# Kernel optimization log

Measured on AMD Instinct MI355X. Metric: run time of the kernel, lower is better.

The kernel has to match this reference:

```python
import jax, jax.numpy as jnp
import numpy as np

B, T, D_MODEL, N_HEADS, N_KV = 2, 2048, 1024, 16, 4
HEAD = D_MODEL // N_HEADS  # 64
NEG_INF = -1e9


def sine_table(features, length):
    # standard RoPE frequency table: theta_i = 10000^(2i/d)
    fraction = jnp.arange(0, features, 2, dtype=jnp.float32) / features
    timescale = 10000.0 ** fraction  # (features/2,)
    sinusoid = jnp.arange(length, dtype=jnp.float32)[:, None] / timescale[None, :]
    sinusoid = jnp.concatenate([sinusoid, sinusoid], axis=-1)  # (L, features)
    return jnp.sin(sinusoid), jnp.cos(sinusoid)


def rotate_half(x):
    x1, x2 = jnp.split(x, 2, axis=-1)
    return jnp.concatenate([-x2, x1], axis=-1)


def apply_rope(x, sin, cos):
    # x: (B, H, T, D); sin/cos: (L, D)
    t = x.shape[-2]
    return x * cos[:t][None, None] + rotate_half(x) * sin[:t][None, None]


def setup_inputs() -> dict:
    key = jax.random.key(0)
    k1, k2, k3, k4 = jax.random.split(key, 4)
    return {
        'q': jax.random.normal(k1, (B, T, D_MODEL), dtype=jnp.float32),
        'k': jax.random.normal(k2, (B, T, N_KV * HEAD), dtype=jnp.float32),
        'v': jax.random.normal(k3, (B, T, N_KV * HEAD), dtype=jnp.float32),
        'w_out': jax.random.normal(k4, (D_MODEL, D_MODEL), dtype=jnp.float32) * 0.02,
    }


def reference(q, k, v, w_out):
    Bq, Tq, C = q.shape
    head = C // N_HEADS
    # split heads: q -> (B, n_heads, T, head); k/v -> (B, n_kv, T, head)
    qh = q.reshape(Bq, Tq, N_HEADS, head).transpose(0, 2, 1, 3)
    kh = k.reshape(Bq, Tq, N_KV, head).transpose(0, 2, 1, 3)
    vh = v.reshape(Bq, Tq, N_KV, head).transpose(0, 2, 1, 3)
    # inline RoPE on q and k
    sin, cos = sine_table(head, Tq)
    qh = apply_rope(qh, sin, cos)
    kh = apply_rope(kh, sin, cos)
    # GQA repeat of kv heads to match q heads
    rep = N_HEADS // N_KV
    kh = jnp.repeat(kh, rep, axis=1)
    vh = jnp.repeat(vh, rep, axis=1)
    # manual scaled-dot-product attention with causal masking (full T^2 logits)
    logits = jnp.einsum('bhqd,bhkd->bhqk', qh, kh) / jnp.sqrt(jnp.float32(head))
    causal = jnp.tril(jnp.ones((Tq, Tq), dtype=jnp.float32))
    logits = jnp.where(causal == 0, NEG_INF, logits)
    attn = jax.nn.softmax(logits, axis=-1)
    out = jnp.einsum('bhqk,bhkd->bhqd', attn, vh)
    out = out.transpose(0, 2, 1, 3).reshape(Bq, Tq, C)
    return out @ w_out
```

## Files before the change

kernel.cpp:

```cpp
#include <hip/hip_runtime.h>
#include <math.h>

#define T_SEQ 2048
#define NH    16
#define NKV   4

typedef __attribute__((ext_vector_type(8))) _Float16 f16x8;
typedef __attribute__((ext_vector_type(4))) _Float16 f16x4;
typedef __attribute__((ext_vector_type(4))) float    f32x4;

__global__ __launch_bounds__(256) void prep_kernel(const float* __restrict__ k,
                                                   const float* __restrict__ v,
                                                   const float* __restrict__ w,
                                                   float2* __restrict__ tb,
                                                   _Float16* __restrict__ Kr,
                                                   _Float16* __restrict__ Vt,
                                                   _Float16* __restrict__ Wt)
{
    __shared__ _Float16 L[64 * 72];
    const int bx = blockIdx.x;
    if (bx < 256) {
        int idx = bx * 256 + threadIdx.x;
        int i = idx & 31, t = idx >> 5;
        float inv = __expf((float)i * (-9.210340371976184f / 32.0f));
        float ang = (float)t * inv;
        tb[idx] = make_float2(cosf(ang), sinf(ang));
    } else if (bx < 2304) {
        int idx = (bx - 256) * 256 + threadIdx.x;
        int i   = idx & 31;
        int t   = (idx >> 5) & 2047;
        int bk  = idx >> 16;
        float inv = __expf((float)i * (-9.210340371976184f / 32.0f));
        float ang = (float)t * inv;
        float sn = sinf(ang), cs = cosf(ang);
        const float* src = k + ((size_t)(bk >> 2) * T_SEQ + t) * 256 + (bk & 3) * 64 + i;
        float x1 = src[0], x2 = src[32];
        _Float16* dst = Kr + ((size_t)bk * T_SEQ + t) * 64 + i;
        dst[0]  = (_Float16)(x1 * cs - x2 * sn);
        dst[32] = (_Float16)(x2 * cs + x1 * sn);
    } else if (bx < 2560) {
        const int id = bx - 2304;
        const int t0 = (id & 31) * 64, bk = id >> 5;
        const int b = bk >> 2, kh = bk & 3;
        const int rr = threadIdx.x >> 2, pp = threadIdx.x & 3;
        const float* src = v + ((size_t)(b * T_SEQ + t0 + rr)) * 256 + kh * 64 + pp * 16;
        f32x4 s0 = *(const f32x4*)(src), s1 = *(const f32x4*)(src + 4);
        f32x4 s2 = *(const f32x4*)(src + 8), s3 = *(const f32x4*)(src + 12);
        _Float16* lp = &L[rr * 72 + pp * 16];
        #pragma unroll
        for (int j = 0; j < 4; ++j) { lp[j] = (_Float16)s0[j]; lp[4+j] = (_Float16)s1[j];
                                      lp[8+j] = (_Float16)s2[j]; lp[12+j] = (_Float16)s3[j]; }
        __syncthreads();
        f16x8 w0, w1;
        #pragma unroll
        for (int j = 0; j < 8; ++j) w0[j] = L[(pp * 16 + j) * 72 + rr];
        #pragma unroll
        for (int j = 0; j < 8; ++j) w1[j] = L[(pp * 16 + 8 + j) * 72 + rr];
        _Float16* dst = Vt + ((size_t)bk * 64 + rr) * T_SEQ + t0 + pp * 16;
        *(f16x8*)dst = w0; *(f16x8*)(dst + 8) = w1;
    } else {
        const int id = bx - 2560;
        const int k0 = (id & 15) * 64, n0 = (id >> 4) * 64;
        const int rr = threadIdx.x >> 2, pp = threadIdx.x & 3;
        const float* src = w + (size_t)(k0 + rr) * 1024 + n0 + pp * 16;
        f32x4 s0 = *(const f32x4*)(src), s1 = *(const f32x4*)(src + 4);
        f32x4 s2 = *(const f32x4*)(src + 8), s3 = *(const f32x4*)(src + 12);
        _Float16* lp = &L[rr * 72 + pp * 16];
        #pragma unroll
        for (int j = 0; j < 4; ++j) { lp[j] = (_Float16)s0[j]; lp[4+j] = (_Float16)s1[j];
                                      lp[8+j] = (_Float16)s2[j]; lp[12+j] = (_Float16)s3[j]; }
        __syncthreads();
        f16x8 w0, w1;
        #pragma unroll
        for (int j = 0; j < 8; ++j) w0[j] = L[(pp * 16 + j) * 72 + rr];
        #pragma unroll
        for (int j = 0; j < 8; ++j) w1[j] = L[(pp * 16 + 8 + j) * 72 + rr];
        _Float16* dst = Wt + (size_t)(n0 + rr) * 1024 + k0 + pp * 16;
        *(f16x8*)dst = w0; *(f16x8*)(dst + 8) = w1;
    }
}


__global__ __launch_bounds__(256) void attn_kernel(const float* __restrict__ q,
                                                   const float2* __restrict__ tb,
                                                   const _Float16* __restrict__ Kr,
                                                   const _Float16* __restrict__ Vt,
                                                   _Float16* __restrict__ AO)
{
    __shared__ _Float16 smem[16384];

    const int wid  = threadIdx.x >> 6;
    const int lane = threadIdx.x & 63;
    const int bh = blockIdx.x & 31;
    const int p  = blockIdx.x >> 5;
    const int qb0 = p, qb1 = 31 - p;
    const int b = bh >> 4, h = bh & 15;
    const int kh = h >> 2;
    const int bkh = b * NKV + kh;
    const int g = lane >> 4, r = lane & 15;

    const int srow   = wid * 16 + (lane >> 3);
    const int schunk = lane & 7;
    const _Float16* kgbase = Kr + (size_t)bkh * T_SEQ * 64;
    const _Float16* vgbase = Vt + (size_t)bkh * 64 * T_SEQ;
    const int kd0 = srow * 64 + ((schunk ^ (srow & 7)) * 8);
    const int kd1 = kd0 + 8 * 64;

    f16x8 stK0, stK1, stV0, stV1;
    {
        const _Float16* kg = kgbase + (size_t)srow * 64 + schunk * 8;
        stK0 = *(const f16x8*)(kg);
        stK1 = *(const f16x8*)(kg + 8 * 64);
        const _Float16* vg = vgbase + (size_t)srow * T_SEQ + schunk * 8;
        stV0 = *(const f16x8*)(vg);
        stV1 = *(const f16x8*)(vg + 8 * T_SEQ);
    }

    f16x8 qa[2][2];
    #pragma unroll
    for (int tl = 0; tl < 2; ++tl) {
        const int t = (tl ? qb1 : qb0) * 64 + wid * 16 + r;
        const float* qs = q + ((size_t)b * T_SEQ + t) * 1024 + h * 64 + 8 * g;
        const float2* tp = tb + t * 32 + 8 * g;
        #pragma unroll
        for (int j = 0; j < 8; ++j) {
            float x0 = qs[j], x1 = qs[32 + j];
            float2 cs = tp[j];
            qa[tl][0][j] = (_Float16)((x0 * cs.x - x1 * cs.y) * 0.125f);
            qa[tl][1][j] = (_Float16)((x1 * cs.x + x0 * cs.y) * 0.125f);
        }
    }

    *(f16x8*)(&smem[kd0])        = stK0;
    *(f16x8*)(&smem[kd1])        = stK1;
    *(f16x8*)(&smem[8192 + kd0]) = stV0;
    *(f16x8*)(&smem[8192 + kd1]) = stV1;
    __syncthreads();

    f32x4 o[2][4];
    f32x4 o4[2];
    #pragma unroll
    for (int tl = 0; tl < 2; ++tl) {
        #pragma unroll
        for (int db = 0; db < 4; ++db) o[tl][db] = (f32x4){0.f,0.f,0.f,0.f};
        o4[tl] = (f32x4){0.f,0.f,0.f,0.f};
    }
    const f16x4 onesf = {(_Float16)1.f, (_Float16)1.f, (_Float16)1.f, (_Float16)1.f};
    float mrun[2] = {-INFINITY, -INFINITY};
    int cur = 0;

    for (int kvb = 0; kvb <= qb1; ++kvb) {
        const bool hasNext = (kvb < qb1);
        if (hasNext) {
            const int nb = (kvb + 1) * 64;
            const _Float16* kg = kgbase + (size_t)(nb + srow) * 64 + schunk * 8;
            stK0 = *(const f16x8*)(kg);
            stK1 = *(const f16x8*)(kg + 8 * 64);
            const _Float16* vg = vgbase + (size_t)srow * T_SEQ + nb + schunk * 8;
            stV0 = *(const f16x8*)(vg);
            stV1 = *(const f16x8*)(vg + 8 * T_SEQ);
        }
        const bool act0 = (kvb <= qb0);
        const _Float16* ks = smem + cur * 4096;
        const _Float16* vs = smem + 8192 + cur * 4096;

        f32x4 stt[2][4];
        __builtin_amdgcn_s_setprio(1);
        #pragma unroll
        for (int kt = 0; kt < 4; ++kt) {
            f16x8 ka0 = *(const f16x8*)(ks + (kt*16 + r) * 64 + ((g       ^ (r & 7)) * 8));
            f16x8 ka1 = *(const f16x8*)(ks + (kt*16 + r) * 64 + (((4 + g) ^ (r & 7)) * 8));
            f32x4 s1 = {0.f,0.f,0.f,0.f};
            s1 = __builtin_amdgcn_mfma_f32_16x16x32_f16(ka0, qa[1][0], s1, 0, 0, 0);
            s1 = __builtin_amdgcn_mfma_f32_16x16x32_f16(ka1, qa[1][1], s1, 0, 0, 0);
            stt[1][kt] = s1;
            if (act0) {
                f32x4 s0 = {0.f,0.f,0.f,0.f};
                s0 = __builtin_amdgcn_mfma_f32_16x16x32_f16(ka0, qa[0][0], s0, 0, 0, 0);
                s0 = __builtin_amdgcn_mfma_f32_16x16x32_f16(ka1, qa[0][1], s0, 0, 0, 0);
                stt[0][kt] = s0;
            }
        }
        __builtin_amdgcn_s_setprio(0);

        if (kvb == qb0) {
            #pragma unroll
            for (int kt = 0; kt < 4; ++kt)
                #pragma unroll
                for (int j = 0; j < 4; ++j)
                    if (kt*16 + 4*g + j > wid*16 + r) stt[0][kt][j] = -1e9f;
        }
        if (kvb == qb1) {
            #pragma unroll
            for (int kt = 0; kt < 4; ++kt)
                #pragma unroll
                for (int j = 0; j < 4; ++j)
                    if (kt*16 + 4*g + j > wid*16 + r) stt[1][kt][j] = -1e9f;
        }

        f16x4 pf[2][4];
        #pragma unroll
        for (int tl = 0; tl < 2; ++tl) {
            if (tl == 0 && !act0) continue;
            float a0 = fmaxf(fmaxf(stt[tl][0][0], stt[tl][0][1]),
                             fmaxf(stt[tl][0][2], stt[tl][0][3]));
            float a1 = fmaxf(fmaxf(stt[tl][1][0], stt[tl][1][1]),
                             fmaxf(stt[tl][1][2], stt[tl][1][3]));
            float a2 = fmaxf(fmaxf(stt[tl][2][0], stt[tl][2][1]),
                             fmaxf(stt[tl][2][2], stt[tl][2][3]));
            float a3 = fmaxf(fmaxf(stt[tl][3][0], stt[tl][3][1]),
                             fmaxf(stt[tl][3][2], stt[tl][3][3]));
            float pmL = fmaxf(fmaxf(a0, a1), fmaxf(a2, a3));
            if (!__all(pmL <= mrun[tl] + 8.0f)) {
                float pm = fmaxf(pmL, __shfl_xor(pmL, 16));
                pm = fmaxf(pm, __shfl_xor(pm, 32));
                float mn   = fmaxf(mrun[tl], pm);
                float corr = __expf(mrun[tl] - mn);
                mrun[tl]   = mn;
                f32x4 cf = { __shfl(corr, 4*g + 0), __shfl(corr, 4*g + 1),
                             __shfl(corr, 4*g + 2), __shfl(corr, 4*g + 3) };
                o[tl][0] *= cf; o[tl][1] *= cf; o[tl][2] *= cf; o[tl][3] *= cf;
                o4[tl]   *= cf;
            }
            #pragma unroll
            for (int kt = 0; kt < 4; ++kt) {
                float p0 = __expf(stt[tl][kt][0] - mrun[tl]);
                float p1 = __expf(stt[tl][kt][1] - mrun[tl]);
                float p2 = __expf(stt[tl][kt][2] - mrun[tl]);
                float p3 = __expf(stt[tl][kt][3] - mrun[tl]);
                pf[tl][kt] = (f16x4){(_Float16)p0, (_Float16)p1,
                                     (_Float16)p2, (_Float16)p3};
            }
        }

        __builtin_amdgcn_s_setprio(1);
        #pragma unroll
        for (int kt = 0; kt < 4; ++kt) {
            const int vc = ((2*kt + (g >> 1)) ^ (r & 7)) * 8 + (g & 1) * 4;
            f16x4 v0 = *(const f16x4*)(vs + (0*16 + r) * 64 + vc);
            f16x4 v1 = *(const f16x4*)(vs + (1*16 + r) * 64 + vc);
            f16x4 v2 = *(const f16x4*)(vs + (2*16 + r) * 64 + vc);
            f16x4 v3 = *(const f16x4*)(vs + (3*16 + r) * 64 + vc);
            o[1][0] = __builtin_amdgcn_mfma_f32_16x16x16f16(pf[1][kt], v0, o[1][0], 0, 0, 0);
            o[1][1] = __builtin_amdgcn_mfma_f32_16x16x16f16(pf[1][kt], v1, o[1][1], 0, 0, 0);
            o[1][2] = __builtin_amdgcn_mfma_f32_16x16x16f16(pf[1][kt], v2, o[1][2], 0, 0, 0);
            o[1][3] = __builtin_amdgcn_mfma_f32_16x16x16f16(pf[1][kt], v3, o[1][3], 0, 0, 0);
            o4[1]   = __builtin_amdgcn_mfma_f32_16x16x16f16(pf[1][kt], onesf, o4[1], 0, 0, 0);
            if (act0) {
                o[0][0] = __builtin_amdgcn_mfma_f32_16x16x16f16(pf[0][kt], v0, o[0][0], 0, 0, 0);
                o[0][1] = __builtin_amdgcn_mfma_f32_16x16x16f16(pf[0][kt], v1, o[0][1], 0, 0, 0);
                o[0][2] = __builtin_amdgcn_mfma_f32_16x16x16f16(pf[0][kt], v2, o[0][2], 0, 0, 0);
                o[0][3] = __builtin_amdgcn_mfma_f32_16x16x16f16(pf[0][kt], v3, o[0][3], 0, 0, 0);
                o4[0]   = __builtin_amdgcn_mfma_f32_16x16x16f16(pf[0][kt], onesf, o4[0], 0, 0, 0);
            }
        }
        __builtin_amdgcn_s_setprio(0);

        if (hasNext) {
            _Float16* kw = smem + (cur ^ 1) * 4096;
            _Float16* vw = smem + 8192 + (cur ^ 1) * 4096;
            *(f16x8*)(&kw[kd0]) = stK0;
            *(f16x8*)(&kw[kd1]) = stK1;
            *(f16x8*)(&vw[kd0]) = stV0;
            *(f16x8*)(&vw[kd1]) = stV1;
            cur ^= 1;
        }
        __syncthreads();
    }

    #pragma unroll
    for (int tl = 0; tl < 2; ++tl) {
        f32x4 li;
        #pragma unroll
        for (int j = 0; j < 4; ++j) li[j] = 1.0f / o4[tl][j];
        _Float16* Os = smem + tl * 4608;
        #pragma unroll
        for (int db = 0; db < 4; ++db) {
            f32x4 ov = o[tl][db] * li;
            #pragma unroll
            for (int j = 0; j < 4; ++j)
                Os[(wid*16 + 4*g + j) * 72 + db*16 + r] = (_Float16)ov[j];
        }
    }
    __syncthreads();
    {
        const int row = threadIdx.x >> 2, part = threadIdx.x & 3;
        #pragma unroll
        for (int tl = 0; tl < 2; ++tl) {
            const int qb = tl ? qb1 : qb0;
            const _Float16* src = smem + tl * 4608 + row * 72 + part * 16;
            _Float16* dst = AO + ((size_t)b * T_SEQ + qb * 64 + row) * 1024 + h * 64 + part * 16;
            *(f16x8*)dst       = *(const f16x8*)src;
            *(f16x8*)(dst + 8) = *(const f16x8*)(src + 8);
        }
    }
}


#define AST 40
__global__ __launch_bounds__(256) void gemm_kernel(const _Float16* __restrict__ A,
                                                   const _Float16* __restrict__ Bt,
                                                   float* __restrict__ C)
{
    __shared__ _Float16 As[2][128 * AST];
    __shared__ _Float16 Bs[2][64 * AST];
    const int tid  = threadIdx.x;
    const int by   = blockIdx.x & 31;
    const int bx   = blockIdx.x >> 5;
    const int lane = tid & 63;
    const int wid  = tid >> 6;
    const int g = lane >> 4, r = lane & 15;
    const int wm = wid >> 1, wn = wid & 1;

    f32x4 acc[4][2];
    #pragma unroll
    for (int i = 0; i < 4; ++i)
        #pragma unroll
        for (int j = 0; j < 2; ++j) acc[i][j] = (f32x4){0.f,0.f,0.f,0.f};

    const int c0 = tid, c1 = tid + 256;
    const size_t a0off = (size_t)(by*128 + (c0 >> 2)) * 1024 + (c0 & 3) * 8;
    const size_t a1off = (size_t)(by*128 + (c1 >> 2)) * 1024 + (c1 & 3) * 8;
    const size_t b0off = (size_t)(bx*64  + (c0 >> 2)) * 1024 + (c0 & 3) * 8;
    const int ad0 = (c0 >> 2) * AST + (c0 & 3) * 8;
    const int ad1 = (c1 >> 2) * AST + (c1 & 3) * 8;

    f16x8 a0 = *(const f16x8*)(A  + a0off);
    f16x8 a1 = *(const f16x8*)(A  + a1off);
    f16x8 b0 = *(const f16x8*)(Bt + b0off);
    *(f16x8*)(&As[0][ad0]) = a0;
    *(f16x8*)(&As[0][ad1]) = a1;
    *(f16x8*)(&Bs[0][ad0]) = b0;
    __syncthreads();
    int cur = 0;

    for (int kt = 0; kt < 32; ++kt) {
        if (kt < 31) {
            a0 = *(const f16x8*)(A  + a0off + (kt+1) * 32);
            a1 = *(const f16x8*)(A  + a1off + (kt+1) * 32);
            b0 = *(const f16x8*)(Bt + b0off + (kt+1) * 32);
        }
        f16x8 af[4], bfv[2];
        #pragma unroll
        for (int mi = 0; mi < 4; ++mi)
            af[mi] = *(const f16x8*)(&As[cur][(wm*64 + mi*16 + r) * AST + 8 * g]);
        #pragma unroll
        for (int ni = 0; ni < 2; ++ni)
            bfv[ni] = *(const f16x8*)(&Bs[cur][(wn*32 + ni*16 + r) * AST + 8 * g]);
        __builtin_amdgcn_s_setprio(1);
        #pragma unroll
        for (int mi = 0; mi < 4; ++mi)
            #pragma unroll
            for (int ni = 0; ni < 2; ++ni)
                acc[mi][ni] = __builtin_amdgcn_mfma_f32_16x16x32_f16(
                                  af[mi], bfv[ni], acc[mi][ni], 0, 0, 0);
        __builtin_amdgcn_s_setprio(0);
        if (kt < 31) {
            *(f16x8*)(&As[cur ^ 1][ad0]) = a0;
            *(f16x8*)(&As[cur ^ 1][ad1]) = a1;
            *(f16x8*)(&Bs[cur ^ 1][ad0]) = b0;
            cur ^= 1;
        }
        __syncthreads();
    }
    #pragma unroll
    for (int mi = 0; mi < 4; ++mi)
        #pragma unroll
        for (int ni = 0; ni < 2; ++ni)
            #pragma unroll
            for (int j = 0; j < 4; ++j)
                C[(size_t)(by*128 + wm*64 + mi*16 + 4*g + j) * 1024
                  + bx*64 + wn*32 + ni*16 + r] = acc[mi][ni][j];
}


extern "C" void kernel_launch(void* const* d_in, const int* in_sizes, int n_in,
                              void* d_out, int out_size, void* d_ws, size_t ws_size,
                              hipStream_t stream) {
    const float* q = (const float*)d_in[0];
    const float* k = (const float*)d_in[1];
    const float* v = (const float*)d_in[2];
    const float* w = (const float*)d_in[3];
    float* out = (float*)d_out;

    char* ws = (char*)d_ws;
    float2*   tb = (float2*)(ws);
    _Float16* Kr = (_Float16*)(ws + ((size_t)1 << 20));
    _Float16* Vt = (_Float16*)(ws + ((size_t)3 << 20));
    _Float16* Wt = (_Float16*)(ws + ((size_t)5 << 20));
    _Float16* AO = (_Float16*)(ws + ((size_t)7 << 20));

    hipLaunchKernelGGL(prep_kernel,  dim3(2816), dim3(256), 0, stream, k, v, w, tb, Kr, Vt, Wt);
    hipLaunchKernelGGL(attn_kernel,  dim3(512),  dim3(256), 0, stream, q, tb, Kr, Vt, AO);
    hipLaunchKernelGGL(gemm_kernel,  dim3(512),  dim3(256), 0, stream, AO, Wt, out);
}
```

Before: 76.72 us.

## Rework attention to 32x32 MFMA tiles with contiguous 128-row query blocks

Replaces the paired-query-block (p, 31-p) scheme with one contiguous 128-row query chunk per block, where each wave handles 32 query rows using 32x32x16 MFMA for both QK^T and PV. The softmax moves to exp2 with log2e folded into the Q scale, and the row sum is accumulated in registers instead of through an extra MFMA against a ones vector. P is packed with cvt_pkrtz and exchanged across lane halves with shuffles to form the A operand. Blocks are launched heaviest-chunk first. The aim is to cut MFMA instruction count and the wasted ones-column work, at the cost of more cross-lane shuffles and less even per-block causal work than the paired scheme.

```diff
diff --git a/kernel.cpp b/kernel.cpp
--- a/kernel.cpp
+++ b/kernel.cpp
@@ -5,9 +5,19 @@
 #define NH    16
 #define NKV   4
 
-typedef __attribute__((ext_vector_type(8))) _Float16 f16x8;
-typedef __attribute__((ext_vector_type(4))) _Float16 f16x4;
-typedef __attribute__((ext_vector_type(4))) float    f32x4;
+typedef __attribute__((ext_vector_type(8)))  _Float16 f16x8;
+typedef __attribute__((ext_vector_type(4)))  _Float16 f16x4;
+typedef __attribute__((ext_vector_type(2)))  __fp16   fp16x2b;
+typedef __attribute__((ext_vector_type(4)))  float    f32x4;
+typedef __attribute__((ext_vector_type(16))) float    f32x16;
+
+#if __has_builtin(__builtin_amdgcn_exp2f)
+#define EXP2F(x) __builtin_amdgcn_exp2f(x)
+#else
+#define EXP2F(x) exp2f(x)
+#endif
+
+#define QSCALE 0.18033688011112042f
 
 __global__ __launch_bounds__(256) void prep_kernel(const float* __restrict__ k,
                                                    const float* __restrict__ v,
@@ -89,15 +99,17 @@
 {
     __shared__ _Float16 smem[16384];
 
-    const int wid  = threadIdx.x >> 6;
-    const int lane = threadIdx.x & 63;
+    const int tid  = threadIdx.x;
+    const int wid  = tid >> 6;
+    const int lane = tid & 63;
     const int bh = blockIdx.x & 31;
-    const int p  = blockIdx.x >> 5;
-    const int qb0 = p, qb1 = 31 - p;
+    const int c  = 15 - (blockIdx.x >> 5);
     const int b = bh >> 4, h = bh & 15;
-    const int kh = h >> 2;
-    const int bkh = b * NKV + kh;
-    const int g = lane >> 4, r = lane & 15;
+    const int bkh = b * NKV + (h >> 2);
+    const int hi = lane >> 5;
+    const int qc = lane & 31;
+    const int qlo = c * 128 + wid * 32;
+    const int tq  = qlo + qc;
 
     const int srow   = wid * 16 + (lane >> 3);
     const int schunk = lane & 7;
@@ -116,18 +128,27 @@
         stV1 = *(const f16x8*)(vg + 8 * T_SEQ);
     }
 
-    f16x8 qa[2][2];
-    #pragma unroll
-    for (int tl = 0; tl < 2; ++tl) {
-        const int t = (tl ? qb1 : qb0) * 64 + wid * 16 + r;
-        const float* qs = q + ((size_t)b * T_SEQ + t) * 1024 + h * 64 + 8 * g;
-        const float2* tp = tb + t * 32 + 8 * g;
-        #pragma unroll
-        for (int j = 0; j < 8; ++j) {
-            float x0 = qs[j], x1 = qs[32 + j];
-            float2 cs = tp[j];
-            qa[tl][0][j] = (_Float16)((x0 * cs.x - x1 * cs.y) * 0.125f);
-            qa[tl][1][j] = (_Float16)((x1 * cs.x + x0 * cs.y) * 0.125f);
+    f16x8 qa[4];
+    {
+        const float* qrow = q + ((size_t)b * T_SEQ + tq) * 1024 + h * 64;
+        float raw[4][8];
+        #pragma unroll
+        for (int ds = 0; ds < 4; ++ds) {
+            f32x4 r0 = *(const f32x4*)(qrow + 16 * ds + 8 * hi);
+            f32x4 r1 = *(const f32x4*)(qrow + 16 * ds + 8 * hi + 4);
+            #pragma unroll
+            for (int j = 0; j < 4; ++j) { raw[ds][j] = r0[j]; raw[ds][4 + j] = r1[j]; }
+        }
+        #pragma unroll
+        for (int ds = 0; ds < 2; ++ds) {
+            const float2* tp = tb + (size_t)tq * 32 + 16 * ds + 8 * hi;
+            #pragma unroll
+            for (int j = 0; j < 8; ++j) {
+                float2 cs = tp[j];
+                float x0 = raw[ds][j], x1 = raw[ds + 2][j];
+                qa[ds][j]     = (_Float16)((x0 * cs.x - x1 * cs.y) * QSCALE);
+                qa[ds + 2][j] = (_Float16)((x1 * cs.x + x0 * cs.y) * QSCALE);
+            }
         }
     }
 
@@ -137,20 +158,15 @@
     *(f16x8*)(&smem[8192 + kd1]) = stV1;
     __syncthreads();
 
-    f32x4 o[2][4];
-    f32x4 o4[2];
+    f32x16 o0, o1;
     #pragma unroll
-    for (int tl = 0; tl < 2; ++tl) {
-        #pragma unroll
-        for (int db = 0; db < 4; ++db) o[tl][db] = (f32x4){0.f,0.f,0.f,0.f};
-        o4[tl] = (f32x4){0.f,0.f,0.f,0.f};
-    }
-    const f16x4 onesf = {(_Float16)1.f, (_Float16)1.f, (_Float16)1.f, (_Float16)1.f};
-    float mrun[2] = {-INFINITY, -INFINITY};
+    for (int i = 0; i < 16; ++i) { o0[i] = 0.f; o1[i] = 0.f; }
+    float mrun = -INFINITY, lsum = 0.0f;
     int cur = 0;
-
-    for (int kvb = 0; kvb <= qb1; ++kvb) {
-        const bool hasNext = (kvb < qb1);
+    const int NT = 2 * c + 2;
+
+    for (int kvb = 0; kvb < NT; ++kvb) {
+        const bool hasNext = (kvb < NT - 1);
         if (hasNext) {
             const int nb = (kvb + 1) * 64;
             const _Float16* kg = kgbase + (size_t)(nb + srow) * 64 + schunk * 8;
@@ -160,101 +176,128 @@
             stV0 = *(const f16x8*)(vg);
             stV1 = *(const f16x8*)(vg + 8 * T_SEQ);
         }
-        const bool act0 = (kvb <= qb0);
         const _Float16* ks = smem + cur * 4096;
         const _Float16* vs = smem + 8192 + cur * 4096;
 
-        f32x4 stt[2][4];
-        __builtin_amdgcn_s_setprio(1);
-        #pragma unroll
-        for (int kt = 0; kt < 4; ++kt) {
-            f16x8 ka0 = *(const f16x8*)(ks + (kt*16 + r) * 64 + ((g       ^ (r & 7)) * 8));
-            f16x8 ka1 = *(const f16x8*)(ks + (kt*16 + r) * 64 + (((4 + g) ^ (r & 7)) * 8));
-            f32x4 s1 = {0.f,0.f,0.f,0.f};
-            s1 = __builtin_amdgcn_mfma_f32_16x16x32_f16(ka0, qa[1][0], s1, 0, 0, 0);
-            s1 = __builtin_amdgcn_mfma_f32_16x16x32_f16(ka1, qa[1][1], s1, 0, 0, 0);
-            stt[1][kt] = s1;
-            if (act0) {
-                f32x4 s0 = {0.f,0.f,0.f,0.f};
-                s0 = __builtin_amdgcn_mfma_f32_16x16x32_f16(ka0, qa[0][0], s0, 0, 0, 0);
-                s0 = __builtin_amdgcn_mfma_f32_16x16x32_f16(ka1, qa[0][1], s0, 0, 0, 0);
-                stt[0][kt] = s0;
-            }
-        }
-        __builtin_amdgcn_s_setprio(0);
-
-        if (kvb == qb0) {
-            #pragma unroll
-            for (int kt = 0; kt < 4; ++kt)
-                #pragma unroll
-                for (int j = 0; j < 4; ++j)
-                    if (kt*16 + 4*g + j > wid*16 + r) stt[0][kt][j] = -1e9f;
-        }
-        if (kvb == qb1) {
-            #pragma unroll
-            for (int kt = 0; kt < 4; ++kt)
-                #pragma unroll
-                for (int j = 0; j < 4; ++j)
-                    if (kt*16 + 4*g + j > wid*16 + r) stt[1][kt][j] = -1e9f;
-        }
-
-        f16x4 pf[2][4];
-        #pragma unroll
-        for (int tl = 0; tl < 2; ++tl) {
-            if (tl == 0 && !act0) continue;
-            float a0 = fmaxf(fmaxf(stt[tl][0][0], stt[tl][0][1]),
-                             fmaxf(stt[tl][0][2], stt[tl][0][3]));
-            float a1 = fmaxf(fmaxf(stt[tl][1][0], stt[tl][1][1]),
-                             fmaxf(stt[tl][1][2], stt[tl][1][3]));
-            float a2 = fmaxf(fmaxf(stt[tl][2][0], stt[tl][2][1]),
-                             fmaxf(stt[tl][2][2], stt[tl][2][3]));
-            float a3 = fmaxf(fmaxf(stt[tl][3][0], stt[tl][3][1]),
-                             fmaxf(stt[tl][3][2], stt[tl][3][3]));
-            float pmL = fmaxf(fmaxf(a0, a1), fmaxf(a2, a3));
-            if (!__all(pmL <= mrun[tl] + 8.0f)) {
-                float pm = fmaxf(pmL, __shfl_xor(pmL, 16));
-                pm = fmaxf(pm, __shfl_xor(pm, 32));
-                float mn   = fmaxf(mrun[tl], pm);
-                float corr = __expf(mrun[tl] - mn);
-                mrun[tl]   = mn;
-                f32x4 cf = { __shfl(corr, 4*g + 0), __shfl(corr, 4*g + 1),
-                             __shfl(corr, 4*g + 2), __shfl(corr, 4*g + 3) };
-                o[tl][0] *= cf; o[tl][1] *= cf; o[tl][2] *= cf; o[tl][3] *= cf;
-                o4[tl]   *= cf;
-            }
-            #pragma unroll
-            for (int kt = 0; kt < 4; ++kt) {
-                float p0 = __expf(stt[tl][kt][0] - mrun[tl]);
-                float p1 = __expf(stt[tl][kt][1] - mrun[tl]);
-                float p2 = __expf(stt[tl][kt][2] - mrun[tl]);
-                float p3 = __expf(stt[tl][kt][3] - mrun[tl]);
-                pf[tl][kt] = (f16x4){(_Float16)p0, (_Float16)p1,
-                                     (_Float16)p2, (_Float16)p3};
-            }
-        }
-
-        __builtin_amdgcn_s_setprio(1);
-        #pragma unroll
-        for (int kt = 0; kt < 4; ++kt) {
-            const int vc = ((2*kt + (g >> 1)) ^ (r & 7)) * 8 + (g & 1) * 4;
-            f16x4 v0 = *(const f16x4*)(vs + (0*16 + r) * 64 + vc);
-            f16x4 v1 = *(const f16x4*)(vs + (1*16 + r) * 64 + vc);
-            f16x4 v2 = *(const f16x4*)(vs + (2*16 + r) * 64 + vc);
-            f16x4 v3 = *(const f16x4*)(vs + (3*16 + r) * 64 + vc);
-            o[1][0] = __builtin_amdgcn_mfma_f32_16x16x16f16(pf[1][kt], v0, o[1][0], 0, 0, 0);
-            o[1][1] = __builtin_amdgcn_mfma_f32_16x16x16f16(pf[1][kt], v1, o[1][1], 0, 0, 0);
-            o[1][2] = __builtin_amdgcn_mfma_f32_16x16x16f16(pf[1][kt], v2, o[1][2], 0, 0, 0);
-            o[1][3] = __builtin_amdgcn_mfma_f32_16x16x16f16(pf[1][kt], v3, o[1][3], 0, 0, 0);
-            o4[1]   = __builtin_amdgcn_mfma_f32_16x16x16f16(pf[1][kt], onesf, o4[1], 0, 0, 0);
-            if (act0) {
-                o[0][0] = __builtin_amdgcn_mfma_f32_16x16x16f16(pf[0][kt], v0, o[0][0], 0, 0, 0);
-                o[0][1] = __builtin_amdgcn_mfma_f32_16x16x16f16(pf[0][kt], v1, o[0][1], 0, 0, 0);
-                o[0][2] = __builtin_amdgcn_mfma_f32_16x16x16f16(pf[0][kt], v2, o[0][2], 0, 0, 0);
-                o[0][3] = __builtin_amdgcn_mfma_f32_16x16x16f16(pf[0][kt], v3, o[0][3], 0, 0, 0);
-                o4[0]   = __builtin_amdgcn_mfma_f32_16x16x16f16(pf[0][kt], onesf, o4[0], 0, 0, 0);
-            }
-        }
-        __builtin_amdgcn_s_setprio(0);
+        const int rel = kvb * 64 - qlo;
+        if (rel <= 0) {
+            const bool act1  = (rel <= -32);
+            f32x16 s0, s1;
+            #pragma unroll
+            for (int i = 0; i < 16; ++i) { s0[i] = 0.f; s1[i] = 0.f; }
+            __builtin_amdgcn_s_setprio(1);
+            {
+                const int krow = qc;
+                const int rsw = krow & 7;
+                #pragma unroll
+                for (int ds = 0; ds < 4; ++ds) {
+                    f16x8 ka = *(const f16x8*)(ks + krow * 64 + (((2*ds + hi) ^ rsw) * 8));
+                    s0 = __builtin_amdgcn_mfma_f32_32x32x16_f16(ka, qa[ds], s0, 0, 0, 0);
+                }
+            }
+            if (act1) {
+                const int krow = 32 + qc;
+                const int rsw = krow & 7;
+                #pragma unroll
+                for (int ds = 0; ds < 4; ++ds) {
+                    f16x8 ka = *(const f16x8*)(ks + krow * 64 + (((2*ds + hi) ^ rsw) * 8));
+                    s1 = __builtin_amdgcn_mfma_f32_32x32x16_f16(ka, qa[ds], s1, 0, 0, 0);
+                }
+            }
+            __builtin_amdgcn_s_setprio(0);
+
+            if (rel == 0) {
+                #pragma unroll
+                for (int r = 0; r < 16; ++r)
+                    if ((r & 3) + 8 * (r >> 2) + 4 * hi > qc) s0[r] = -1e30f;
+            }
+            if (act1 && rel == -32) {
+                #pragma unroll
+                for (int r = 0; r < 16; ++r)
+                    if ((r & 3) + 8 * (r >> 2) + 4 * hi > qc) s1[r] = -1e30f;
+            }
+
+            float pmL = s0[0];
+            #pragma unroll
+            for (int r = 1; r < 16; ++r) pmL = fmaxf(pmL, s0[r]);
+            if (act1) {
+                #pragma unroll
+                for (int r = 0; r < 16; ++r) pmL = fmaxf(pmL, s1[r]);
+            }
+            if (!__all(pmL <= mrun + 8.0f)) {
+                float pm = fmaxf(pmL, __shfl_xor(pmL, 32));
+                float mn = fmaxf(mrun, pm);
+                float corr = EXP2F(mrun - mn);
+                mrun = mn;
+                lsum *= corr;
+                #pragma unroll
+                for (int r = 0; r < 16; ++r) {
+                    float cfr = __shfl(corr, (r & 3) + 8 * (r >> 2) + 4 * hi);
+                    o0[r] *= cfr; o1[r] *= cfr;
+                }
+            }
+
+            unsigned pk0[8], pk1[8];
+            float ps = 0.0f;
+            #pragma unroll
+            for (int i = 0; i < 8; ++i) {
+                float p0 = EXP2F(s0[2*i]     - mrun);
+                float p1 = EXP2F(s0[2*i + 1] - mrun);
+                ps += p0 + p1;
+                union { fp16x2b h; unsigned u; } cv;
+                cv.h = __builtin_amdgcn_cvt_pkrtz(p0, p1);
+                pk0[i] = cv.u;
+            }
+            if (act1) {
+                #pragma unroll
+                for (int i = 0; i < 8; ++i) {
+                    float p0 = EXP2F(s1[2*i]     - mrun);
+                    float p1 = EXP2F(s1[2*i + 1] - mrun);
+                    ps += p0 + p1;
+                    union { fp16x2b h; unsigned u; } cv;
+                    cv.h = __builtin_amdgcn_cvt_pkrtz(p0, p1);
+                    pk1[i] = cv.u;
+                }
+            }
+            lsum += ps;
+
+            union { unsigned u[4]; f16x8 v; } af[4];
+            {
+                unsigned t0 = (unsigned)__shfl_xor((int)(hi ? pk0[0] : pk0[2]), 32);
+                unsigned t1 = (unsigned)__shfl_xor((int)(hi ? pk0[1] : pk0[3]), 32);
+                unsigned t2 = (unsigned)__shfl_xor((int)(hi ? pk0[4] : pk0[6]), 32);
+                unsigned t3 = (unsigned)__shfl_xor((int)(hi ? pk0[5] : pk0[7]), 32);
+                af[0].u[0] = hi ? t0 : pk0[0]; af[0].u[1] = hi ? t1 : pk0[1];
+                af[0].u[2] = hi ? pk0[2] : t0; af[0].u[3] = hi ? pk0[3] : t1;
+                af[1].u[0] = hi ? t2 : pk0[4]; af[1].u[1] = hi ? t3 : pk0[5];
+                af[1].u[2] = hi ? pk0[6] : t2; af[1].u[3] = hi ? pk0[7] : t3;
+            }
+            if (act1) {
+                unsigned t0 = (unsigned)__shfl_xor((int)(hi ? pk1[0] : pk1[2]), 32);
+                unsigned t1 = (unsigned)__shfl_xor((int)(hi ? pk1[1] : pk1[3]), 32);
+                unsigned t2 = (unsigned)__shfl_xor((int)(hi ? pk1[4] : pk1[6]), 32);
+                unsigned t3 = (unsigned)__shfl_xor((int)(hi ? pk1[5] : pk1[7]), 32);
+                af[2].u[0] = hi ? t0 : pk1[0]; af[2].u[1] = hi ? t1 : pk1[1];
+                af[2].u[2] = hi ? pk1[2] : t0; af[2].u[3] = hi ? pk1[3] : t1;
+                af[3].u[0] = hi ? t2 : pk1[4]; af[3].u[1] = hi ? t3 : pk1[5];
+                af[3].u[2] = hi ? pk1[6] : t2; af[3].u[3] = hi ? pk1[7] : t3;
+            }
+
+            __builtin_amdgcn_s_setprio(1);
+            const int nkc = act1 ? 4 : 2;
+            #pragma unroll
+            for (int kc = 0; kc < 4; ++kc) {
+                if (kc < nkc) {
+                    const int vr0 = qc;
+                    const int vr1 = 32 + qc;
+                    f16x8 vb0 = *(const f16x8*)(vs + vr0 * 64 + (((2*kc + hi) ^ (vr0 & 7)) * 8));
+                    f16x8 vb1 = *(const f16x8*)(vs + vr1 * 64 + (((2*kc + hi) ^ (vr1 & 7)) * 8));
+                    o0 = __builtin_amdgcn_mfma_f32_32x32x16_f16(af[kc].v, vb0, o0, 0, 0, 0);
+                    o1 = __builtin_amdgcn_mfma_f32_32x32x16_f16(af[kc].v, vb1, o1, 0, 0, 0);
+                }
+            }
+            __builtin_amdgcn_s_setprio(0);
+        }
 
         if (hasNext) {
             _Float16* kw = smem + (cur ^ 1) * 4096;
@@ -268,31 +311,26 @@
         __syncthreads();
     }
 
-    #pragma unroll
-    for (int tl = 0; tl < 2; ++tl) {
-        f32x4 li;
-        #pragma unroll
-        for (int j = 0; j < 4; ++j) li[j] = 1.0f / o4[tl][j];
-        _Float16* Os = smem + tl * 4608;
-        #pragma unroll
-        for (int db = 0; db < 4; ++db) {
-            f32x4 ov = o[tl][db] * li;
-            #pragma unroll
-            for (int j = 0; j < 4; ++j)
-                Os[(wid*16 + 4*g + j) * 72 + db*16 + r] = (_Float16)ov[j];
+    lsum += __shfl_xor(lsum, 32);
+    const float li = 1.0f / lsum;
+    {
+        _Float16* Os = smem;
+        #pragma unroll
+        for (int r = 0; r < 16; ++r) {
+            const int crow = (r & 3) + 8 * (r >> 2) + 4 * hi;
+            float lir = __shfl(li, crow);
+            Os[(wid * 32 + crow) * 72 + qc]      = (_Float16)(o0[r] * lir);
+            Os[(wid * 32 + crow) * 72 + 32 + qc] = (_Float16)(o1[r] * lir);
         }
     }
     __syncthreads();
     {
-        const int row = threadIdx.x >> 2, part = threadIdx.x & 3;
-        #pragma unroll
-        for (int tl = 0; tl < 2; ++tl) {
-            const int qb = tl ? qb1 : qb0;
-            const _Float16* src = smem + tl * 4608 + row * 72 + part * 16;
-            _Float16* dst = AO + ((size_t)b * T_SEQ + qb * 64 + row) * 1024 + h * 64 + part * 16;
-            *(f16x8*)dst       = *(const f16x8*)src;
-            *(f16x8*)(dst + 8) = *(const f16x8*)(src + 8);
-        }
+        const int row = tid >> 1, part = tid & 1;
+        const _Float16* src = smem + row * 72 + part * 32;
+        _Float16* dst = AO + ((size_t)b * T_SEQ + c * 128 + row) * 1024 + h * 64 + part * 32;
+        #pragma unroll
+        for (int j = 0; j < 4; ++j)
+            *(f16x8*)(dst + j * 8) = *(const f16x8*)(src + j * 8);
     }
 }
 
```

Measured after the change: 82.39 us. 7.4% more time.

## Prefetch KV two tiles ahead and batch K RoPE prep per thread

Applied to the files above, without the earlier changes.

The attention loop now prefetches K/V global loads two tiles ahead, using two register staging sets that alternate through an unrolled lambda. Each iteration ends in a lightweight LDS-only barrier (waitcnt lgkmcnt plus s_barrier) instead of __syncthreads. The prep kernel's K RoPE section has each thread loop over all 8 batch-head pairs and reuse one sin/cos computation, shrinking the grid from 2816 to 1024 blocks. This hides more global-load latency and removes redundant trig work, at the cost of extra registers that may lower occupancy.

```diff
diff --git a/kernel.cpp b/kernel.cpp
--- a/kernel.cpp
+++ b/kernel.cpp
@@ -5,9 +5,17 @@
 #define NH    16
 #define NKV   4
 
-typedef __attribute__((ext_vector_type(8))) _Float16 f16x8;
-typedef __attribute__((ext_vector_type(4))) _Float16 f16x4;
-typedef __attribute__((ext_vector_type(4))) float    f32x4;
+typedef __attribute__((ext_vector_type(8)))  _Float16 f16x8;
+typedef __attribute__((ext_vector_type(4)))  _Float16 f16x4;
+typedef __attribute__((ext_vector_type(4)))  float    f32x4;
+
+#define LDS_BARRIER()                                        \
+    do {                                                     \
+        __builtin_amdgcn_sched_barrier(0);                   \
+        asm volatile("s_waitcnt lgkmcnt(0)" ::: "memory");   \
+        __builtin_amdgcn_s_barrier();                        \
+        __builtin_amdgcn_sched_barrier(0);                   \
+    } while (0)
 
 __global__ __launch_bounds__(256) void prep_kernel(const float* __restrict__ k,
                                                    const float* __restrict__ v,
@@ -25,21 +33,23 @@
         float inv = __expf((float)i * (-9.210340371976184f / 32.0f));
         float ang = (float)t * inv;
         tb[idx] = make_float2(cosf(ang), sinf(ang));
-    } else if (bx < 2304) {
+    } else if (bx < 512) {
         int idx = (bx - 256) * 256 + threadIdx.x;
         int i   = idx & 31;
-        int t   = (idx >> 5) & 2047;
-        int bk  = idx >> 16;
+        int t   = idx >> 5;
         float inv = __expf((float)i * (-9.210340371976184f / 32.0f));
         float ang = (float)t * inv;
         float sn = sinf(ang), cs = cosf(ang);
-        const float* src = k + ((size_t)(bk >> 2) * T_SEQ + t) * 256 + (bk & 3) * 64 + i;
-        float x1 = src[0], x2 = src[32];
-        _Float16* dst = Kr + ((size_t)bk * T_SEQ + t) * 64 + i;
-        dst[0]  = (_Float16)(x1 * cs - x2 * sn);
-        dst[32] = (_Float16)(x2 * cs + x1 * sn);
-    } else if (bx < 2560) {
-        const int id = bx - 2304;
+        #pragma unroll
+        for (int bk = 0; bk < 8; ++bk) {
+            const float* src = k + ((size_t)(bk >> 2) * T_SEQ + t) * 256 + (bk & 3) * 64 + i;
+            float x1 = src[0], x2 = src[32];
+            _Float16* dst = Kr + ((size_t)bk * T_SEQ + t) * 64 + i;
+            dst[0]  = (_Float16)(x1 * cs - x2 * sn);
+            dst[32] = (_Float16)(x2 * cs + x1 * sn);
+        }
+    } else if (bx < 768) {
+        const int id = bx - 512;
         const int t0 = (id & 31) * 64, bk = id >> 5;
         const int b = bk >> 2, kh = bk & 3;
         const int rr = threadIdx.x >> 2, pp = threadIdx.x & 3;
@@ -59,7 +69,7 @@
         _Float16* dst = Vt + ((size_t)bk * 64 + rr) * T_SEQ + t0 + pp * 16;
         *(f16x8*)dst = w0; *(f16x8*)(dst + 8) = w1;
     } else {
-        const int id = bx - 2560;
+        const int id = bx - 768;
         const int k0 = (id & 15) * 64, n0 = (id >> 4) * 64;
         const int rr = threadIdx.x >> 2, pp = threadIdx.x & 3;
         const float* src = w + (size_t)(k0 + rr) * 1024 + n0 + pp * 16;
@@ -98,6 +108,7 @@
     const int kh = h >> 2;
     const int bkh = b * NKV + kh;
     const int g = lane >> 4, r = lane & 15;
+    const int NT = qb1 + 1;
 
     const int srow   = wid * 16 + (lane >> 3);
     const int schunk = lane & 7;
@@ -106,14 +117,14 @@
     const int kd0 = srow * 64 + ((schunk ^ (srow & 7)) * 8);
     const int kd1 = kd0 + 8 * 64;
 
-    f16x8 stK0, stK1, stV0, stV1;
+    f16x8 sAK0, sAK1, sAV0, sAV1, sBK0, sBK1, sBV0, sBV1;
     {
         const _Float16* kg = kgbase + (size_t)srow * 64 + schunk * 8;
-        stK0 = *(const f16x8*)(kg);
-        stK1 = *(const f16x8*)(kg + 8 * 64);
+        sAK0 = *(const f16x8*)(kg);
+        sAK1 = *(const f16x8*)(kg + 8 * 64);
         const _Float16* vg = vgbase + (size_t)srow * T_SEQ + schunk * 8;
-        stV0 = *(const f16x8*)(vg);
-        stV1 = *(const f16x8*)(vg + 8 * T_SEQ);
+        sAV0 = *(const f16x8*)(vg);
+        sAV1 = *(const f16x8*)(vg + 8 * T_SEQ);
     }
 
     f16x8 qa[2][2];
@@ -131,11 +142,19 @@
         }
     }
 
-    *(f16x8*)(&smem[kd0])        = stK0;
-    *(f16x8*)(&smem[kd1])        = stK1;
-    *(f16x8*)(&smem[8192 + kd0]) = stV0;
-    *(f16x8*)(&smem[8192 + kd1]) = stV1;
-    __syncthreads();
+    *(f16x8*)(&smem[kd0])        = sAK0;
+    *(f16x8*)(&smem[kd1])        = sAK1;
+    *(f16x8*)(&smem[8192 + kd0]) = sAV0;
+    *(f16x8*)(&smem[8192 + kd1]) = sAV1;
+    {
+        const _Float16* kg = kgbase + (size_t)(64 + srow) * 64 + schunk * 8;
+        sBK0 = *(const f16x8*)(kg);
+        sBK1 = *(const f16x8*)(kg + 8 * 64);
+        const _Float16* vg = vgbase + (size_t)srow * T_SEQ + 64 + schunk * 8;
+        sBV0 = *(const f16x8*)(vg);
+        sBV1 = *(const f16x8*)(vg + 8 * T_SEQ);
+    }
+    LDS_BARRIER();
 
     f32x4 o[2][4];
     f32x4 o4[2];
@@ -147,22 +166,22 @@
     }
     const f16x4 onesf = {(_Float16)1.f, (_Float16)1.f, (_Float16)1.f, (_Float16)1.f};
     float mrun[2] = {-INFINITY, -INFINITY};
-    int cur = 0;
-
-    for (int kvb = 0; kvb <= qb1; ++kvb) {
-        const bool hasNext = (kvb < qb1);
-        if (hasNext) {
-            const int nb = (kvb + 1) * 64;
+
+    auto tile_body = [&](int kvb,
+                         f16x8& iK0, f16x8& iK1, f16x8& iV0, f16x8& iV1,
+                         f16x8& oK0, f16x8& oK1, f16x8& oV0, f16x8& oV1) {
+        if (kvb + 2 < NT) {
+            const int nb = (kvb + 2) * 64;
             const _Float16* kg = kgbase + (size_t)(nb + srow) * 64 + schunk * 8;
-            stK0 = *(const f16x8*)(kg);
-            stK1 = *(const f16x8*)(kg + 8 * 64);
+            iK0 = *(const f16x8*)(kg);
+            iK1 = *(const f16x8*)(kg + 8 * 64);
             const _Float16* vg = vgbase + (size_t)srow * T_SEQ + nb + schunk * 8;
-            stV0 = *(const f16x8*)(vg);
-            stV1 = *(const f16x8*)(vg + 8 * T_SEQ);
+            iV0 = *(const f16x8*)(vg);
+            iV1 = *(const f16x8*)(vg + 8 * T_SEQ);
         }
         const bool act0 = (kvb <= qb0);
-        const _Float16* ks = smem + cur * 4096;
-        const _Float16* vs = smem + 8192 + cur * 4096;
+        const _Float16* ks = smem + (kvb & 1) * 4096;
+        const _Float16* vs = smem + 8192 + (kvb & 1) * 4096;
 
         f32x4 stt[2][4];
         __builtin_amdgcn_s_setprio(1);
@@ -256,16 +275,21 @@
         }
         __builtin_amdgcn_s_setprio(0);
 
-        if (hasNext) {
-            _Float16* kw = smem + (cur ^ 1) * 4096;
-            _Float16* vw = smem + 8192 + (cur ^ 1) * 4096;
-            *(f16x8*)(&kw[kd0]) = stK0;
-            *(f16x8*)(&kw[kd1]) = stK1;
-            *(f16x8*)(&vw[kd0]) = stV0;
-            *(f16x8*)(&vw[kd1]) = stV1;
-            cur ^= 1;
-        }
-        __syncthreads();
+        if (kvb + 1 < NT) {
+            _Float16* kw = smem + ((kvb + 1) & 1) * 4096;
+            _Float16* vw = smem + 8192 + ((kvb + 1) & 1) * 4096;
+            *(f16x8*)(&kw[kd0]) = oK0;
+            *(f16x8*)(&kw[kd1]) = oK1;
+            *(f16x8*)(&vw[kd0]) = oV0;
+            *(f16x8*)(&vw[kd1]) = oV1;
+        }
+        LDS_BARRIER();
+    };
+
+    for (int t = 0; t < NT; ) {
+        tile_body(t, sAK0, sAK1, sAV0, sAV1, sBK0, sBK1, sBV0, sBV1); ++t;
+        if (t >= NT) break;
+        tile_body(t, sBK0, sBK1, sBV0, sBV1, sAK0, sAK1, sAV0, sAV1); ++t;
     }
 
     #pragma unroll
@@ -390,7 +414,7 @@
     _Float16* Wt = (_Float16*)(ws + ((size_t)5 << 20));
     _Float16* AO = (_Float16*)(ws + ((size_t)7 << 20));
 
-    hipLaunchKernelGGL(prep_kernel,  dim3(2816), dim3(256), 0, stream, k, v, w, tb, Kr, Vt, Wt);
+    hipLaunchKernelGGL(prep_kernel,  dim3(1024), dim3(256), 0, stream, k, v, w, tb, Kr, Vt, Wt);
     hipLaunchKernelGGL(attn_kernel,  dim3(512),  dim3(256), 0, stream, q, tb, Kr, Vt, AO);
     hipLaunchKernelGGL(gemm_kernel,  dim3(512),  dim3(256), 0, stream, AO, Wt, out);
 }
```

Measured after the change: 77.96 us. Within noise of the previous version (+1.6%).
